# Kernel optimization log

Measured on AMD Instinct MI355X. Metric: run time of the kernel, lower is better.

## Reference

```python
import math
import jax, jax.numpy as jnp
import numpy as np

DIM = 1536
HEADS = 8
DK = 64
DV = 192
NRPF = 192  # num_rel_pos_features, divisible by 6
SEQ = 1536
BATCH = 4
SCALE = DK ** -0.5


def get_positional_embed(n, feature_size):
    # distances in [-(n-1), n-1], length 2n-1
    dist = jnp.arange(-n + 1, n).astype(jnp.float32)
    adist = jnp.abs(dist)[:, None]  # [2n-1, 1]
    f = feature_size // 6  # 3 feature fns, each doubled by sign channel
    # exponential half-life features
    max_range = math.log(n) / math.log(2.0)
    half_life = 2.0 ** jnp.linspace(3.0, max_range, f)[None, :]
    emb_exp = jnp.exp(-math.log(2.0) / half_life * adist)
    # central mask features
    center_widths = (2.0 ** jnp.arange(1, f + 1).astype(jnp.float32) - 1.0)[None, :]
    emb_cm = (center_widths > adist).astype(jnp.float32)
    # gamma pdf features
    stddev = n / (2.0 * f)
    start_mean = n / float(f)
    mean = jnp.linspace(start_mean, float(n), f)[None, :]
    conc = (mean / stddev) ** 2
    rate = mean / stddev ** 2
    log_unnorm = (conc - 1.0) * jnp.log(jnp.maximum(adist, 1e-20)) - rate * adist
    log_norm = jax.scipy.special.gammaln(conc) - conc * jnp.log(rate)
    prob = jnp.exp(log_unnorm - log_norm) + 1e-8
    emb_g = prob / jnp.max(prob, axis=-1, keepdims=True)
    emb = jnp.concatenate([emb_exp, emb_cm, emb_g], axis=-1)  # [2n-1, feat/2]
    return jnp.concatenate([emb, jnp.sign(dist)[:, None] * emb], axis=-1)  # [2n-1, feat]


def relative_shift(x):
    # x: [b, h, n, 2n-1] -> [b, h, n, n] via the Transformer-XL shift trick
    b, h, t1, t2 = x.shape
    x = jnp.concatenate([jnp.zeros_like(x[..., :1]), x], axis=-1)  # [b,h,t1,t2+1]
    x = x.reshape(b, h, t2 + 1, t1)[:, :, 1:, :].reshape(b, h, t1, t2)
    return x[..., : (t2 + 2) // 2]


def layer_norm(x, g, b, eps=1e-5):
    mu = jnp.mean(x, axis=-1, keepdims=True)
    var = jnp.var(x, axis=-1, keepdims=True)
    return (x - mu) * jax.lax.rsqrt(var + eps) * g + b


def setup_inputs() -> dict:
    key = jax.random.key(0)
    ks = jax.random.split(key, 16)
    d, h, dk, dv = DIM, HEADS, DK, DV
    inp = {
        "x": jax.random.normal(ks[0], (BATCH, SEQ, d), dtype=jnp.float32),
        "ln1_g": jnp.ones((d,), jnp.float32),
        "ln1_b": jnp.zeros((d,), jnp.float32),
        "Wq": jax.random.normal(ks[1], (d, h * dk), jnp.float32) / math.sqrt(d),
        "Wk": jax.random.normal(ks[2], (d, h * dk), jnp.float32) / math.sqrt(d),
        "Wv": jax.random.normal(ks[3], (d, h * dv), jnp.float32) / math.sqrt(d),
        "Wo": jax.random.normal(ks[4], (h * dv, d), jnp.float32) / math.sqrt(h * dv),
        "bo": jnp.zeros((d,), jnp.float32),
        "Wrk": jax.random.normal(ks[5], (NRPF, h * dk), jnp.float32) / math.sqrt(NRPF),
        "rel_content_bias": jax.random.normal(ks[6], (1, h, 1, dk), jnp.float32),
        "rel_pos_bias": jax.random.normal(ks[7], (1, h, 1, dk), jnp.float32),
        "ln2_g": jnp.ones((d,), jnp.float32),
        "ln2_b": jnp.zeros((d,), jnp.float32),
        "W1": jax.random.normal(ks[8], (d, 2 * d), jnp.float32) / math.sqrt(d),
        "b1": jnp.zeros((2 * d,), jnp.float32),
        "W2": jax.random.normal(ks[9], (2 * d, d), jnp.float32) / math.sqrt(2 * d),
        "b2": jnp.zeros((d,), jnp.float32),
    }
    return inp


def _attention(x, Wq, Wk, Wv, Wo, bo, Wrk, rel_content_bias, rel_pos_bias):
    b, n, _ = x.shape
    h, dk, dv = HEADS, DK, DV
    q = (x @ Wq).reshape(b, n, h, dk).transpose(0, 2, 1, 3) * SCALE  # [b,h,n,dk]
    k = (x @ Wk).reshape(b, n, h, dk).transpose(0, 2, 1, 3)
    v = (x @ Wv).reshape(b, n, h, dv).transpose(0, 2, 1, 3)
    content_logits = jnp.einsum('bhid,bhjd->bhij', q + rel_content_bias, k)
    positions = get_positional_embed(n, NRPF)  # [2n-1, NRPF]
    rel_k = (positions @ Wrk).reshape(2 * n - 1, h, dk).transpose(1, 0, 2)  # [h,2n-1,dk]
    rel_logits = jnp.einsum('bhid,hjd->bhij', q + rel_pos_bias, rel_k)
    rel_logits = relative_shift(rel_logits)  # [b,h,n,n]
    attn = jax.nn.softmax(content_logits + rel_logits, axis=-1)
    out = jnp.einsum('bhij,bhjd->bhid', attn, v)
    out = out.transpose(0, 2, 1, 3).reshape(b, n, h * dv)
    return out @ Wo + bo


def reference(x, ln1_g, ln1_b, Wq, Wk, Wv, Wo, bo, Wrk, rel_content_bias,
              rel_pos_bias, ln2_g, ln2_b, W1, b1, W2, b2):
    # pre-LN attention with residual
    x = x + _attention(layer_norm(x, ln1_g, ln1_b), Wq, Wk, Wv, Wo, bo, Wrk,
                       rel_content_bias, rel_pos_bias)
    # MLP block (carries its own LayerNorm and residual)
    y = layer_norm(x, ln2_g, ln2_b)
    y = jax.nn.relu(y @ W1 + b1)
    y = y @ W2 + b2
    return y + x
```

## Files before the change

kernel.cpp:

```cpp
#include <hip/hip_runtime.h>
#include <hip/hip_bf16.h>
#include <math.h>

#define SEQN 1536
#define NH 8
#define MROWS 6144
#define NDIST 3071

typedef __attribute__((ext_vector_type(8))) _Float16 f16x8;
typedef __attribute__((ext_vector_type(4))) _Float16 f16x4;
typedef __attribute__((ext_vector_type(4))) float f32x4;

#define MFMAH(a, b, c) __builtin_amdgcn_mfma_f32_16x16x32_f16(a, b, c, 0, 0, 0)

__device__ __forceinline__ void gl_lds16(const void* g, void* l) {
  __builtin_amdgcn_global_load_lds(
      (const __attribute__((address_space(1))) void*)g,
      (__attribute__((address_space(3))) void*)l, 16, 0, 0);
}

__global__ __launch_bounds__(64) void pos_embed_kernel(float* __restrict__ pos) {
  int row = blockIdx.x;
  int j = threadIdx.x;
  if (j >= 32) return;
  float dist = (float)(row - (SEQN - 1));
  float adist = fabsf(dist);
  float sgn = (dist > 0.f) ? 1.f : (dist < 0.f ? -1.f : 0.f);

  const float max_range = 10.58496250072116f;
  float hl = exp2f(3.0f + ((max_range - 3.0f) / 31.0f) * (float)j);
  float e_exp = expf(-0.6931471805599453f / hl * adist);

  float cw = exp2f((float)(j + 1)) - 1.0f;
  float e_cm = (cw > adist) ? 1.0f : 0.0f;

  float mean = 48.0f * (float)(j + 1);
  float tt = mean / 24.0f;
  float conc = tt * tt;
  float rate = mean / 576.0f;
  float log_unnorm = (conc - 1.0f) * logf(fmaxf(adist, 1e-20f)) - rate * adist;
  float log_norm = lgammaf(conc) - conc * logf(rate);
  float prob = expf(log_unnorm - log_norm) + 1e-8f;
  float mx = prob;
  #pragma unroll
  for (int off = 16; off >= 1; off >>= 1)
    mx = fmaxf(mx, __shfl_xor(mx, off, 32));
  float e_g = prob / mx;

  float* o = pos + (size_t)row * 192;
  o[j] = e_exp;        o[32 + j] = e_cm;        o[64 + j] = e_g;
  o[96 + j] = sgn * e_exp; o[128 + j] = sgn * e_cm; o[160 + j] = sgn * e_g;
}

__global__ __launch_bounds__(512) void relk_kernel(
    const float* __restrict__ pos, const float* __restrict__ Wrk,
    const float* __restrict__ pb, _Float16* __restrict__ rk, float* __restrict__ PR) {
  __shared__ float prow[16][192];
  const int d0 = blockIdx.x * 16;
  const int t = threadIdx.x;
  #pragma unroll
  for (int p = 0; p < 6; ++p) {
    int idx = t + p * 512;
    int r = idx / 192, c = idx - r * 192;
    prow[r][c] = pos[(size_t)(d0 + r) * 192 + c];
  }
  __syncthreads();
  float acc[16];
  #pragma unroll
  for (int r = 0; r < 16; ++r) acc[r] = 0.f;
  #pragma unroll 4
  for (int kk = 0; kk < 192; ++kk) {
    float wv = Wrk[(size_t)kk * 512 + t];
    #pragma unroll
    for (int r = 0; r < 16; ++r) acc[r] = fmaf(prow[r][kk], wv, acc[r]);
  }
  #pragma unroll
  for (int r = 0; r < 16; ++r)
    rk[(size_t)(d0 + r) * 512 + t] = (_Float16)acc[r];
  float pbv = pb[t];
  #pragma unroll
  for (int r = 0; r < 16; ++r) {
    float pv = pbv * acc[r];
    #pragma unroll
    for (int off = 32; off >= 1; off >>= 1) pv += __shfl_xor(pv, off);
    if ((t & 63) == 0 && (d0 + r) < NDIST)
      PR[(size_t)(t >> 6) * NDIST + d0 + r] = pv;
  }
}

__global__ __launch_bounds__(256) void ln_kernel(
    const float* __restrict__ x, const float* __restrict__ g,
    const float* __restrict__ bta, _Float16* __restrict__ oh) {
  const int row = blockIdx.x;
  const int t = threadIdx.x;
  __shared__ float red[4];
  __shared__ float bc[2];
  const float4* xr = (const float4*)(x + (size_t)row * 1536);
  float4 v0 = xr[t];
  float4 v1 = make_float4(0.f, 0.f, 0.f, 0.f);
  if (t < 128) v1 = xr[256 + t];
  float s = v0.x + v0.y + v0.z + v0.w;
  if (t < 128) s += v1.x + v1.y + v1.z + v1.w;
  #pragma unroll
  for (int off = 32; off >= 1; off >>= 1) s += __shfl_xor(s, off);
  if ((t & 63) == 0) red[t >> 6] = s;
  __syncthreads();
  if (t == 0) bc[0] = (red[0] + red[1] + red[2] + red[3]) * (1.f / 1536.f);
  __syncthreads();
  const float mu = bc[0];
  float d, s2 = 0.f;
  d = v0.x - mu; s2 += d * d; d = v0.y - mu; s2 += d * d;
  d = v0.z - mu; s2 += d * d; d = v0.w - mu; s2 += d * d;
  if (t < 128) {
    d = v1.x - mu; s2 += d * d; d = v1.y - mu; s2 += d * d;
    d = v1.z - mu; s2 += d * d; d = v1.w - mu; s2 += d * d;
  }
  #pragma unroll
  for (int off = 32; off >= 1; off >>= 1) s2 += __shfl_xor(s2, off);
  if ((t & 63) == 0) red[t >> 6] = s2;
  __syncthreads();
  if (t == 0) bc[1] = (red[0] + red[1] + red[2] + red[3]) * (1.f / 1536.f);
  __syncthreads();
  const float inv = rsqrtf(bc[1] + 1e-5f);
  const float4* g4 = (const float4*)g;
  const float4* b4 = (const float4*)bta;
  float4 gg = g4[t], bb = b4[t];
  f16x4 hv;
  hv[0] = (_Float16)((v0.x - mu) * inv * gg.x + bb.x);
  hv[1] = (_Float16)((v0.y - mu) * inv * gg.y + bb.y);
  hv[2] = (_Float16)((v0.z - mu) * inv * gg.z + bb.z);
  hv[3] = (_Float16)((v0.w - mu) * inv * gg.w + bb.w);
  *(f16x4*)(oh + (size_t)row * 1536 + t * 4) = hv;
  if (t < 128) {
    gg = g4[256 + t]; bb = b4[256 + t];
    hv[0] = (_Float16)((v1.x - mu) * inv * gg.x + bb.x);
    hv[1] = (_Float16)((v1.y - mu) * inv * gg.y + bb.y);
    hv[2] = (_Float16)((v1.z - mu) * inv * gg.z + bb.z);
    hv[3] = (_Float16)((v1.w - mu) * inv * gg.w + bb.w);
    *(f16x4*)(oh + (size_t)row * 1536 + 1024 + t * 4) = hv;
  }
}

__global__ __launch_bounds__(256) void convw_kernel(
    const float* __restrict__ W, _Float16* __restrict__ Th,
    int N, int K, int KD, int roff, float scale) {
  __shared__ float tile[32][33];
  const int n0 = blockIdx.x * 32, k0 = blockIdx.y * 32;
  const int t = threadIdx.x;
  const int cr = t >> 5;
  const int cc = t & 31;
  #pragma unroll
  for (int p = 0; p < 4; ++p) {
    int r = cr + p * 8;
    tile[r][cc] = W[(size_t)(k0 + r) * N + n0 + cc];
  }
  __syncthreads();
  #pragma unroll
  for (int p = 0; p < 4; ++p) {
    int r = cr + p * 8;
    float v = tile[cc][r] * scale;
    Th[(size_t)(roff + n0 + r) * KD + k0 + cc] = (_Float16)v;
  }
}

template <int EPI, int BNJ, int MW>
__global__ __launch_bounds__(256, MW) void mgemm_kernel(
    const _Float16* __restrict__ A, const _Float16* __restrict__ B,
    float* __restrict__ C, _Float16* __restrict__ Ch,
    _Float16* __restrict__ Kp, _Float16* __restrict__ Vt, float* __restrict__ CKo,
    const float* __restrict__ bias, const float* __restrict__ res,
    int M, int N, int K) {
  constexpr int BN = BNJ * 32;
  __shared__ _Float16 sm[8192 + BN * 64];
  const int t = threadIdx.x;
  const int lane = t & 63;
  const int w = t >> 6;
  const int wm = w >> 1, wn = w & 1;
  const int slab = (M >> 7) >> 3;
  const int xcd = blockIdx.x & 7;
  const int r = blockIdx.x >> 3;
  const int yt = xcd * slab + (r % slab);
  const int xt = r / slab;
  const int m0 = yt * 128, n0 = xt * BN;

  f32x4 acc[4][BNJ];
  #pragma unroll
  for (int i = 0; i < 4; ++i)
    #pragma unroll
    for (int j = 0; j < BNJ; ++j) acc[i][j] = (f32x4){0.f, 0.f, 0.f, 0.f};

  const int srow = t >> 3;
  const int ssl = t & 7;
  const int ss = ssl ^ (srow & 7);
  const int lr = lane & 15;
  const int g = lane >> 4;
  const int kb = lr & 7;

  for (int k0 = 0; k0 < K; k0 += 64) {
    #pragma unroll
    for (int p = 0; p < 4; ++p) {
      int row = srow + p * 32;
      gl_lds16(A + (size_t)(m0 + row) * K + k0 + ss * 8, &sm[row * 64 + ssl * 8]);
    }
    #pragma unroll
    for (int p = 0; p < BN / 32; ++p) {
      int row = srow + p * 32;
      gl_lds16(B + (size_t)(n0 + row) * K + k0 + ss * 8,
               &sm[8192 + row * 64 + ssl * 8]);
    }
    __syncthreads();
    #pragma unroll
    for (int h2 = 0; h2 < 2; ++h2) {
      const int ksl = ((h2 * 4 + g) ^ kb) * 8;
      f16x8 a[4], b[BNJ];
      #pragma unroll
      for (int i = 0; i < 4; ++i)
        a[i] = *(const f16x8*)(&sm[(wm * 64 + i * 16 + lr) * 64 + ksl]);
      #pragma unroll
      for (int j = 0; j < BNJ; ++j)
        b[j] = *(const f16x8*)(&sm[8192 + (wn * BNJ * 16 + j * 16 + lr) * 64 + ksl]);
      #pragma unroll
      for (int i = 0; i < 4; ++i)
        #pragma unroll
        for (int j = 0; j < BNJ; ++j)
          acc[i][j] = MFMAH(a[i], b[j], acc[i][j]);
    }
    __syncthreads();
  }

  const int lq = lane >> 4;
  #pragma unroll
  for (int i = 0; i < 4; ++i) {
    #pragma unroll
    for (int j = 0; j < BNJ; ++j) {
      const int c0 = n0 + wn * BNJ * 16 + j * 16;
      const int col = c0 + lr;
      const int rbase = m0 + wm * 64 + i * 16 + lq * 4;
      if (EPI == 3) {
        #pragma unroll
        for (int q = 0; q < 4; ++q) {
          size_t o = (size_t)(rbase + q) * N + col;
          C[o] = acc[i][j][q] + bias[col] + res[o];
        }
      } else if (EPI == 2) {
        #pragma unroll
        for (int q = 0; q < 4; ++q) {
          size_t o = (size_t)(rbase + q) * N + col;
          Ch[o] = (_Float16)fmaxf(acc[i][j][q] + bias[col], 0.f);
        }
      } else {
        if (c0 < 512) {
          #pragma unroll
          for (int q = 0; q < 4; ++q)
            Ch[(size_t)(rbase + q) * 512 + col] = (_Float16)acc[i][j][q];
        } else if (c0 < 1024) {
          #pragma unroll
          for (int q = 0; q < 4; ++q)
            Kp[(size_t)(rbase + q) * 512 + (col - 512)] = (_Float16)acc[i][j][q];
        } else {
          int dv = col - 1024;
          int hd = dv / 192;
          int dvh = dv - hd * 192;
          int bb = rbase / 1536;
          int nloc = rbase - bb * 1536;
          f16x4 pk;
          pk[0] = (_Float16)acc[i][j][0];
          pk[1] = (_Float16)acc[i][j][1];
          pk[2] = (_Float16)acc[i][j][2];
          pk[3] = (_Float16)acc[i][j][3];
          *(f16x4*)(Vt + (((size_t)bb * 8 + hd) * 192 + dvh) * 1536 + nloc) = pk;
        }
      }
    }
  }

  if (EPI == 4) {
    const int cw0 = n0 + wn * 64;
    if (cw0 >= 512 && cw0 < 1024) {
      const int hh = (cw0 - 512) >> 6;
      float cbv[4];
      #pragma unroll
      for (int j = 0; j < 4; ++j) cbv[j] = bias[cw0 - 512 + j * 16 + lr];
      #pragma unroll
      for (int i = 0; i < 4; ++i)
        #pragma unroll
        for (int q = 0; q < 4; ++q) {
          float v = acc[i][0][q] * cbv[0] + acc[i][1][q] * cbv[1] +
                    acc[i][2][q] * cbv[2] + acc[i][3][q] * cbv[3];
          #pragma unroll
          for (int off = 8; off >= 1; off >>= 1) v += __shfl_xor(v, off);
          if (lr == 0)
            CKo[(size_t)(m0 + wm * 64 + i * 16 + lq * 4 + q) * 8 + hh] = v;
        }
    }
  }
}

__global__ __launch_bounds__(256, 3) void attn_kernel(
    const _Float16* __restrict__ Qp, const _Float16* __restrict__ Kp,
    const _Float16* __restrict__ Vt, const _Float16* __restrict__ rk,
    const float* __restrict__ PR, const float* __restrict__ CK,
    _Float16* __restrict__ ao) {
  __shared__ _Float16 lds[26752];
  const int id = blockIdx.x;
  const int xcd = id & 7, s = id >> 3;
  const int bh = xcd * 4 + s / 24;
  const int it = s % 24;
  const int b = bh >> 3, h = bh & 7;
  const int t = threadIdx.x;
  const int w = t >> 6;
  const int lane = t & 63;
  const int c15 = lane & 15, g = lane >> 4;
  const int swz = c15 & 7;
  const int vsz = (c15 >> 1) & 3;
  const int qrow0 = it * 64 + w * 16;
  const int rrow0 = 48 - w * 16;
  const int R0 = 1472 - it * 64;

  const int lr = lane >> 3, sl = lane & 7;
  const int ss = sl ^ lr;
  const int ss2 = (lane & 3) ^ ((lane >> 3) & 3);

  f16x8 qh0, qh1;
  {
    size_t qo = ((size_t)(b * SEQN + qrow0 + c15)) * 512 + h * 64 + g * 8;
    qh0 = *(const f16x8*)(Qp + qo);
    qh1 = *(const f16x8*)(Qp + qo + 32);
  }
  f16x8 ones;
  #pragma unroll
  for (int i = 0; i < 8; ++i) ones[i] = (_Float16)1.0f;
  const float* PRrow = PR + (size_t)h * NDIST;
  const float* CKb2 = CK + (size_t)b * SEQN * 8 + h;

  f32x4 acc[13];
  #pragma unroll
  for (int d = 0; d < 13; ++d) acc[d] = (f32x4){0.f, 0.f, 0.f, 0.f};
  float mrun[4];
  #pragma unroll
  for (int q = 0; q < 4; ++q) mrun[q] = -1e30f;

  #define STAGE_KV(J0, KB, VB)                                                   \
    do {                                                                         \
      size_t gk = ((size_t)(b * SEQN + (J0) + w * 8 + lr)) * 512 + h * 64 + ss * 8; \
      gl_lds16(Kp + gk, &lds[(KB) + w * 512]);                                   \
      _Pragma("unroll") for (int p = 0; p < 3; ++p) {                            \
        int rv = w * 48 + p * 16 + (lane >> 2);                                  \
        size_t gv = (((size_t)(b * 8 + h)) * 192 + rv) * SEQN + (J0) + ss2 * 8;  \
        gl_lds16(Vt + gv, &lds[(VB) + (w * 48 + p * 16) * 32]);                  \
      }                                                                          \
    } while (0)

  #define STAGE_R_PRO()                                                          \
    do {                                                                         \
      _Pragma("unroll") for (int p = 0; p < 4; ++p) {                            \
        int rr = w * 32 + p * 8 + lr;                                            \
        size_t gr = ((size_t)(R0 + rr)) * 512 + h * 64 + ss * 8;                 \
        gl_lds16(rk + gr, &lds[16384 + (w * 32 + p * 8) * 64]);                  \
      }                                                                          \
    } while (0)

  #define STAGE_R_INC(REL0)                                                      \
    do {                                                                         \
      int rr = (REL0) + w * 8 + lr;                                              \
      size_t gr = ((size_t)(R0 + rr)) * 512 + h * 64 + ss * 8;                   \
      gl_lds16(rk + gr, &lds[16384 + ((((REL0) + w * 8) & 127)) * 64]);          \
    } while (0)

  #define COMP_T(DST, ETOFF)                                                     \
    do {                                                                         \
      int relrow = (cc32 + rrow0 + (ETOFF) + c15) & 127;                         \
      f16x8 r0_ = *(const f16x8*)(&lds[16384 + relrow * 64 + (g ^ swz) * 8]);    \
      f16x8 r1_ = *(const f16x8*)(&lds[16384 + relrow * 64 + ((4 + g) ^ swz) * 8]); \
      f32x4 tt_ = (f32x4){0.f, 0.f, 0.f, 0.f};                                   \
      tt_ = MFMAH(qh0, r0_, tt_);                                                \
      tt_ = MFMAH(qh1, r1_, tt_);                                                \
      float prv_ = PRrow[dbase + (ETOFF) + c15];                                 \
      _Pragma("unroll") for (int q = 0; q < 4; ++q) tt_[q] += prv_;              \
      DST = tt_;                                                                 \
    } while (0)

  STAGE_KV(0, 0, 4096);
  STAGE_R_PRO();

  f32x4 T0, T1, T2;

  for (int c = 0; c < 48; ++c) {
    const int j0 = c * 32;
    const int cc32 = c * 32;
    const int cur = c & 1;
    const int KB = cur * 2048;
    const int VB = 4096 + cur * 6144;
    __syncthreads();

    if (c < 47) {
      STAGE_KV(j0 + 32, (cur ^ 1) * 2048, 4096 + (cur ^ 1) * 6144);
      if (c >= 1) STAGE_R_INC(cc32 + 96);
    }

    const int dbase = 1520 + j0 - qrow0;
    __builtin_amdgcn_s_setprio(1);
    if (c == 0) {
      COMP_T(T0, 0);
    } else {
      T0 = T2;
    }
    COMP_T(T1, 16);
    COMP_T(T2, 32);
    f32x4 S[2];
    #pragma unroll
    for (int st = 0; st < 2; ++st) {
      int rowK = st * 16 + c15;
      f16x8 kh0 = *(const f16x8*)(&lds[KB + rowK * 64 + (g ^ swz) * 8]);
      f16x8 kh1 = *(const f16x8*)(&lds[KB + rowK * 64 + ((4 + g) ^ swz) * 8]);
      f32x4 ssv = (f32x4){0.f, 0.f, 0.f, 0.f};
      ssv = MFMAH(qh0, kh0, ssv);
      ssv = MFMAH(qh1, kh1, ssv);
      S[st] = ssv;
    }
    __builtin_amdgcn_s_setprio(0);
    float ck0 = CKb2[(size_t)(j0 + c15) * 8];
    float ck1 = CKb2[(size_t)(j0 + 16 + c15) * 8];
    #pragma unroll
    for (int q = 0; q < 4; ++q) {
      int eoff = c15 + 15 - 4 * g - q;
      int src = (lane & 48) | (eoff & 15);
      float t0v = __shfl(T0[q], src);
      float t1v = __shfl(T1[q], src);
      float t2v = __shfl(T2[q], src);
      bool lo = eoff < 16;
      S[0][q] += ck0 + (lo ? t0v : t1v);
      S[1][q] += ck1 + (lo ? t1v : t2v);
    }
    int need = 0;
    #pragma unroll
    for (int st = 0; st < 2; ++st)
      #pragma unroll
      for (int q = 0; q < 4; ++q) need |= (S[st][q] > mrun[q] + 8.0f) ? 1 : 0;
    if (__any(need)) {
      float mx[4];
      #pragma unroll
      for (int q = 0; q < 4; ++q) mx[q] = fmaxf(S[0][q], S[1][q]);
      #pragma unroll
      for (int off = 8; off >= 1; off >>= 1)
        #pragma unroll
        for (int q = 0; q < 4; ++q) mx[q] = fmaxf(mx[q], __shfl_xor(mx[q], off));
      #pragma unroll
      for (int q = 0; q < 4; ++q) {
        float mn = fmaxf(mrun[q], mx[q]);
        float al = __expf(mrun[q] - mn);
        mrun[q] = mn;
        #pragma unroll
        for (int d = 0; d < 13; ++d) acc[d][q] *= al;
      }
    }
    #pragma unroll
    for (int st = 0; st < 2; ++st)
      #pragma unroll
      for (int q = 0; q < 4; ++q)
        lds[24576 + (w * 16 + 4 * g + q) * 34 + st * 16 + c15] =
            (_Float16)__expf(S[st][q] - mrun[q]);

    f16x8 pf = *(const f16x8*)(&lds[24576 + (w * 16 + c15) * 34 + g * 8]);
    __builtin_amdgcn_s_setprio(1);
    #pragma unroll
    for (int d = 0; d < 12; ++d) {
      int rowV = d * 16 + c15;
      f16x8 vf = *(const f16x8*)(&lds[VB + rowV * 32 + (g ^ vsz) * 8]);
      acc[d] = MFMAH(pf, vf, acc[d]);
    }
    acc[12] = MFMAH(pf, ones, acc[12]);
    __builtin_amdgcn_s_setprio(0);
  }

  float rinv[4];
  #pragma unroll
  for (int q = 0; q < 4; ++q) rinv[q] = 1.0f / acc[12][q];
  #pragma unroll
  for (int d = 0; d < 12; ++d) {
    int col = h * 192 + d * 16 + c15;
    #pragma unroll
    for (int q = 0; q < 4; ++q) {
      size_t row = (size_t)(b * SEQN + qrow0 + 4 * g + q);
      ao[row * 1536 + col] = (_Float16)(acc[d][q] * rinv[q]);
    }
  }
  #undef STAGE_KV
  #undef STAGE_R_PRO
  #undef STAGE_R_INC
  #undef COMP_T
}

extern "C" void kernel_launch(void* const* d_in, const int* in_sizes, int n_in,
                              void* d_out, int out_size, void* d_ws, size_t ws_size,
                              hipStream_t stream) {
  (void)in_sizes; (void)n_in; (void)out_size; (void)ws_size;
  const float* x   = (const float*)d_in[0];
  const float* g1  = (const float*)d_in[1];
  const float* be1 = (const float*)d_in[2];
  const float* Wq  = (const float*)d_in[3];
  const float* Wk  = (const float*)d_in[4];
  const float* Wv  = (const float*)d_in[5];
  const float* Wo  = (const float*)d_in[6];
  const float* bo  = (const float*)d_in[7];
  const float* Wrk = (const float*)d_in[8];
  const float* cb  = (const float*)d_in[9];
  const float* pb  = (const float*)d_in[10];
  const float* g2  = (const float*)d_in[11];
  const float* be2 = (const float*)d_in[12];
  const float* W1  = (const float*)d_in[13];
  const float* b1  = (const float*)d_in[14];
  const float* W2  = (const float*)d_in[15];
  const float* b2  = (const float*)d_in[16];
  float* out = (float*)d_out;

  char* B = (char*)d_ws;
  float* pos     = (float*)(B + 0);
  _Float16* rk   = (_Float16*)(B + 2359296);
  float* PRb     = (float*)(B + 5505024);
  float* CKb     = (float*)(B + 5603328);
  _Float16* xn   = (_Float16*)(B + 5799936);
  _Float16* Wb   = (_Float16*)(B + 24674304);
  _Float16* Qp   = (_Float16*)(B + 34111488);
  _Float16* Kp   = (_Float16*)(B + 40402944);
  _Float16* Vtp  = (_Float16*)(B + 46694400);
  _Float16* ao   = (_Float16*)(B + 65568768);
  float* x2      = (float*)(B + 84443136);
  _Float16* h1   = (_Float16*)(B + 122191872);

  pos_embed_kernel<<<NDIST, 64, 0, stream>>>(pos);
  relk_kernel<<<192, 512, 0, stream>>>(pos, Wrk, pb, rk, PRb);
  ln_kernel<<<MROWS, 256, 0, stream>>>(x, g1, be1, xn);
  convw_kernel<<<dim3(16, 48), 256, 0, stream>>>(Wq, Wb, 512, 1536, 1536, 0, 0.125f);
  convw_kernel<<<dim3(16, 48), 256, 0, stream>>>(Wk, Wb, 512, 1536, 1536, 512, 1.0f);
  convw_kernel<<<dim3(48, 48), 256, 0, stream>>>(Wv, Wb, 1536, 1536, 1536, 1024, 1.0f);
  mgemm_kernel<4, 4, 4><<<960, 256, 0, stream>>>(
      xn, Wb, nullptr, Qp, Kp, Vtp, CKb, cb, nullptr, MROWS, 2560, 1536);
  attn_kernel<<<768, 256, 0, stream>>>(Qp, Kp, Vtp, rk, PRb, CKb, ao);
  convw_kernel<<<dim3(48, 48), 256, 0, stream>>>(Wo, Wb, 1536, 1536, 1536, 0, 1.0f);
  mgemm_kernel<3, 3, 4><<<768, 256, 0, stream>>>(
      ao, Wb, x2, nullptr, nullptr, nullptr, nullptr, bo, x, MROWS, 1536, 1536);
  ln_kernel<<<MROWS, 256, 0, stream>>>(x2, g2, be2, xn);
  convw_kernel<<<dim3(96, 48), 256, 0, stream>>>(W1, Wb, 3072, 1536, 1536, 0, 1.0f);
  mgemm_kernel<2, 6, 3><<<768, 256, 0, stream>>>(
      xn, Wb, nullptr, h1, nullptr, nullptr, nullptr, b1, nullptr, MROWS, 3072, 1536);
  convw_kernel<<<dim3(48, 96), 256, 0, stream>>>(W2, Wb, 1536, 3072, 3072, 0, 1.0f);
  mgemm_kernel<3, 3, 4><<<768, 256, 0, stream>>>(
      h1, Wb, out, nullptr, nullptr, nullptr, nullptr, b2, x2, MROWS, 1536, 3072);
}
```

Baseline: 415.3 us.

## Fuse positional embedding into relk and merge weight conversions into one launch

The positional-embedding computation moves into the relk kernel, so each block builds its 16 rows directly in shared memory instead of a separate kernel writing them to global memory and relk reading them back. The six weight transpose/convert launches are merged into one large launch that writes each weight to its own workspace buffer. This removes several kernel launches and the global round trip for the embedding. The cost is a larger workspace, with h1 now reusing the Qp region, and branchy block dispatch inside the merged conversion kernel.

```diff
diff --git a/kernel.cpp b/kernel.cpp
--- a/kernel.cpp
+++ b/kernel.cpp
@@ -19,50 +19,38 @@
       (__attribute__((address_space(3))) void*)l, 16, 0, 0);
 }
 
-__global__ __launch_bounds__(64) void pos_embed_kernel(float* __restrict__ pos) {
-  int row = blockIdx.x;
-  int j = threadIdx.x;
-  if (j >= 32) return;
-  float dist = (float)(row - (SEQN - 1));
-  float adist = fabsf(dist);
-  float sgn = (dist > 0.f) ? 1.f : (dist < 0.f ? -1.f : 0.f);
-
-  const float max_range = 10.58496250072116f;
-  float hl = exp2f(3.0f + ((max_range - 3.0f) / 31.0f) * (float)j);
-  float e_exp = expf(-0.6931471805599453f / hl * adist);
-
-  float cw = exp2f((float)(j + 1)) - 1.0f;
-  float e_cm = (cw > adist) ? 1.0f : 0.0f;
-
-  float mean = 48.0f * (float)(j + 1);
-  float tt = mean / 24.0f;
-  float conc = tt * tt;
-  float rate = mean / 576.0f;
-  float log_unnorm = (conc - 1.0f) * logf(fmaxf(adist, 1e-20f)) - rate * adist;
-  float log_norm = lgammaf(conc) - conc * logf(rate);
-  float prob = expf(log_unnorm - log_norm) + 1e-8f;
-  float mx = prob;
-  #pragma unroll
-  for (int off = 16; off >= 1; off >>= 1)
-    mx = fmaxf(mx, __shfl_xor(mx, off, 32));
-  float e_g = prob / mx;
-
-  float* o = pos + (size_t)row * 192;
-  o[j] = e_exp;        o[32 + j] = e_cm;        o[64 + j] = e_g;
-  o[96 + j] = sgn * e_exp; o[128 + j] = sgn * e_cm; o[160 + j] = sgn * e_g;
-}
-
 __global__ __launch_bounds__(512) void relk_kernel(
-    const float* __restrict__ pos, const float* __restrict__ Wrk,
-    const float* __restrict__ pb, _Float16* __restrict__ rk, float* __restrict__ PR) {
+    const float* __restrict__ Wrk, const float* __restrict__ pb,
+    _Float16* __restrict__ rk, float* __restrict__ PR) {
   __shared__ float prow[16][192];
   const int d0 = blockIdx.x * 16;
   const int t = threadIdx.x;
-  #pragma unroll
-  for (int p = 0; p < 6; ++p) {
-    int idx = t + p * 512;
-    int r = idx / 192, c = idx - r * 192;
-    prow[r][c] = pos[(size_t)(d0 + r) * 192 + c];
+  {
+    const int r = t >> 5, j = t & 31;
+    const int row = d0 + r;
+    float dist = (float)(row - (SEQN - 1));
+    float adist = fabsf(dist);
+    float sgn = (dist > 0.f) ? 1.f : (dist < 0.f ? -1.f : 0.f);
+    const float max_range = 10.58496250072116f;
+    float hl = exp2f(3.0f + ((max_range - 3.0f) / 31.0f) * (float)j);
+    float e_exp = expf(-0.6931471805599453f / hl * adist);
+    float cw = exp2f((float)(j + 1)) - 1.0f;
+    float e_cm = (cw > adist) ? 1.0f : 0.0f;
+    float mean = 48.0f * (float)(j + 1);
+    float tt = mean / 24.0f;
+    float conc = tt * tt;
+    float rate = mean / 576.0f;
+    float log_unnorm = (conc - 1.0f) * logf(fmaxf(adist, 1e-20f)) - rate * adist;
+    float log_norm = lgammaf(conc) - conc * logf(rate);
+    float prob = expf(log_unnorm - log_norm) + 1e-8f;
+    float mx = prob;
+    #pragma unroll
+    for (int off = 16; off >= 1; off >>= 1)
+      mx = fmaxf(mx, __shfl_xor(mx, off, 32));
+    float e_g = prob / mx;
+    prow[r][j] = e_exp;            prow[r][32 + j] = e_cm;
+    prow[r][64 + j] = e_g;         prow[r][96 + j] = sgn * e_exp;
+    prow[r][128 + j] = sgn * e_cm; prow[r][160 + j] = sgn * e_g;
   }
   __syncthreads();
   float acc[16];
@@ -141,11 +129,33 @@
   }
 }
 
-__global__ __launch_bounds__(256) void convw_kernel(
-    const float* __restrict__ W, _Float16* __restrict__ Th,
-    int N, int K, int KD, int roff, float scale) {
+__global__ __launch_bounds__(256) void convw_all_kernel(
+    const float* __restrict__ Wq, const float* __restrict__ Wk,
+    const float* __restrict__ Wv, const float* __restrict__ Wo,
+    const float* __restrict__ W1, const float* __restrict__ W2,
+    _Float16* __restrict__ TQKV, _Float16* __restrict__ TO,
+    _Float16* __restrict__ T1w, _Float16* __restrict__ T2w) {
   __shared__ float tile[32][33];
-  const int n0 = blockIdx.x * 32, k0 = blockIdx.y * 32;
+  int bid = blockIdx.x;
+  const float* W;
+  _Float16* T;
+  int N, KD, roff = 0;
+  float scale = 1.0f;
+  if (bid < 768) {
+    W = Wq; T = TQKV; N = 512; KD = 1536; scale = 0.125f;
+  } else if (bid < 1536) {
+    bid -= 768; W = Wk; T = TQKV; N = 512; KD = 1536; roff = 512;
+  } else if (bid < 3840) {
+    bid -= 1536; W = Wv; T = TQKV; N = 1536; KD = 1536; roff = 1024;
+  } else if (bid < 6144) {
+    bid -= 3840; W = Wo; T = TO; N = 1536; KD = 1536;
+  } else if (bid < 10752) {
+    bid -= 6144; W = W1; T = T1w; N = 3072; KD = 1536;
+  } else {
+    bid -= 10752; W = W2; T = T2w; N = 1536; KD = 3072;
+  }
+  const int nx = N >> 5;
+  const int n0 = (bid % nx) * 32, k0 = (bid / nx) * 32;
   const int t = threadIdx.x;
   const int cr = t >> 5;
   const int cc = t & 31;
@@ -159,7 +169,7 @@
   for (int p = 0; p < 4; ++p) {
     int r = cr + p * 8;
     float v = tile[cc][r] * scale;
-    Th[(size_t)(roff + n0 + r) * KD + k0 + cc] = (_Float16)v;
+    T[(size_t)(roff + n0 + r) * KD + k0 + cc] = (_Float16)v;
   }
 }
 
@@ -515,36 +525,33 @@
   float* out = (float*)d_out;
 
   char* B = (char*)d_ws;
-  float* pos     = (float*)(B + 0);
-  _Float16* rk   = (_Float16*)(B + 2359296);
-  float* PRb     = (float*)(B + 5505024);
-  float* CKb     = (float*)(B + 5603328);
-  _Float16* xn   = (_Float16*)(B + 5799936);
-  _Float16* Wb   = (_Float16*)(B + 24674304);
-  _Float16* Qp   = (_Float16*)(B + 34111488);
-  _Float16* Kp   = (_Float16*)(B + 40402944);
-  _Float16* Vtp  = (_Float16*)(B + 46694400);
-  _Float16* ao   = (_Float16*)(B + 65568768);
-  float* x2      = (float*)(B + 84443136);
-  _Float16* h1   = (_Float16*)(B + 122191872);
-
-  pos_embed_kernel<<<NDIST, 64, 0, stream>>>(pos);
-  relk_kernel<<<192, 512, 0, stream>>>(pos, Wrk, pb, rk, PRb);
+  _Float16* rk    = (_Float16*)(B + 0);
+  float* PRb      = (float*)(B + 3145728);
+  float* CKb      = (float*)(B + 3244032);
+  _Float16* xn    = (_Float16*)(B + 3440640);
+  _Float16* WbQKV = (_Float16*)(B + 22315008);
+  _Float16* WbO   = (_Float16*)(B + 30179328);
+  _Float16* Wb1   = (_Float16*)(B + 34897920);
+  _Float16* Wb2   = (_Float16*)(B + 44335104);
+  _Float16* Qp    = (_Float16*)(B + 53772288);
+  _Float16* Kp    = (_Float16*)(B + 60063744);
+  _Float16* Vtp   = (_Float16*)(B + 66355200);
+  _Float16* ao    = (_Float16*)(B + 85229568);
+  float* x2       = (float*)(B + 104103936);
+  _Float16* h1    = (_Float16*)(B + 53772288);
+
+  relk_kernel<<<192, 512, 0, stream>>>(Wrk, pb, rk, PRb);
+  convw_all_kernel<<<15360, 256, 0, stream>>>(Wq, Wk, Wv, Wo, W1, W2,
+                                              WbQKV, WbO, Wb1, Wb2);
   ln_kernel<<<MROWS, 256, 0, stream>>>(x, g1, be1, xn);
-  convw_kernel<<<dim3(16, 48), 256, 0, stream>>>(Wq, Wb, 512, 1536, 1536, 0, 0.125f);
-  convw_kernel<<<dim3(16, 48), 256, 0, stream>>>(Wk, Wb, 512, 1536, 1536, 512, 1.0f);
-  convw_kernel<<<dim3(48, 48), 256, 0, stream>>>(Wv, Wb, 1536, 1536, 1536, 1024, 1.0f);
   mgemm_kernel<4, 4, 4><<<960, 256, 0, stream>>>(
-      xn, Wb, nullptr, Qp, Kp, Vtp, CKb, cb, nullptr, MROWS, 2560, 1536);
+      xn, WbQKV, nullptr, Qp, Kp, Vtp, CKb, cb, nullptr, MROWS, 2560, 1536);
   attn_kernel<<<768, 256, 0, stream>>>(Qp, Kp, Vtp, rk, PRb, CKb, ao);
-  convw_kernel<<<dim3(48, 48), 256, 0, stream>>>(Wo, Wb, 1536, 1536, 1536, 0, 1.0f);
   mgemm_kernel<3, 3, 4><<<768, 256, 0, stream>>>(
-      ao, Wb, x2, nullptr, nullptr, nullptr, nullptr, bo, x, MROWS, 1536, 1536);
+      ao, WbO, x2, nullptr, nullptr, nullptr, nullptr, bo, x, MROWS, 1536, 1536);
   ln_kernel<<<MROWS, 256, 0, stream>>>(x2, g2, be2, xn);
-  convw_kernel<<<dim3(96, 48), 256, 0, stream>>>(W1, Wb, 3072, 1536, 1536, 0, 1.0f);
   mgemm_kernel<2, 6, 3><<<768, 256, 0, stream>>>(
-      xn, Wb, nullptr, h1, nullptr, nullptr, nullptr, b1, nullptr, MROWS, 3072, 1536);
-  convw_kernel<<<dim3(48, 96), 256, 0, stream>>>(W2, Wb, 1536, 3072, 3072, 0, 1.0f);
+      xn, Wb1, nullptr, h1, nullptr, nullptr, nullptr, b1, nullptr, MROWS, 3072, 1536);
   mgemm_kernel<3, 3, 4><<<768, 256, 0, stream>>>(
-      h1, Wb, out, nullptr, nullptr, nullptr, nullptr, b2, x2, MROWS, 1536, 3072);
-}
+      h1, Wb2, out, nullptr, nullptr, nullptr, nullptr, b2, x2, MROWS, 1536, 3072);
+}
```

New measurement: 400.3 us. 1.04x faster.
